# Kernel optimization log

Measured on AMD Instinct MI355X. Metric: run time of the kernel, lower is better.

Reference implementation:

```python
import jax, jax.numpy as jnp
import numpy as np

N_NODES = 8192
N_EDGES = 262144
D_IN = 512
D_OUT = 512


def setup_inputs() -> dict:
    key = jax.random.key(0)
    k1, k2, k3 = jax.random.split(key, 3)
    x = jax.random.normal(k1, (N_NODES, D_IN), dtype=jnp.float32)
    edge_index = jax.random.randint(k2, (2, N_EDGES), 0, N_NODES, dtype=jnp.int64)
    weight = jax.random.normal(k3, (D_IN, D_OUT), dtype=jnp.float32)
    bias = jnp.zeros((D_OUT,), dtype=jnp.float32)
    return {"x": x, "edge_index": edge_index, "weight": weight, "bias": bias}


def reference(x, edge_index, weight, bias):
    # GCN layer with selfloop=True branch of the original module.
    n = x.shape[0]
    # Dense symmetric adjacency via scatter-set, matching adj[ei0,ei1]=1; adj[ei1,ei0]=1
    adj = jnp.zeros((n, n), dtype=x.dtype)
    adj = adj.at[edge_index[0], edge_index[1]].set(1.0)
    adj = adj.at[edge_index[1], edge_index[0]].set(1.0)
    # Add self loops, symmetric degree normalization D^{-1/2} A D^{-1/2}
    adj = adj + jnp.eye(n, dtype=x.dtype)
    deg = jnp.sum(adj, axis=1)
    dinv = 1.0 / jnp.sqrt(deg)
    adj = adj * dinv[:, None] * dinv[None, :]  # == D @ adj @ D (diagonal scaling)
    return adj @ (x @ weight) + bias
```

## Files before the change

### kernel.cpp

```cpp
#include <hip/hip_runtime.h>
#include <hip/hip_bf16.h>


#define ELL_STRIDE 128

typedef __attribute__((ext_vector_type(8))) short bf16x8;
typedef __attribute__((ext_vector_type(4))) float f32x4;

__device__ __forceinline__ unsigned short f2bf(float f) {
  unsigned u = __float_as_uint(f);
  u = (u + 0x7fff + ((u >> 16) & 1)) >> 16;
  return (unsigned short)u;
}
__device__ __forceinline__ float bflo(unsigned u) {
  return __uint_as_float(u << 16);
}
__device__ __forceinline__ float bfhi(unsigned u) {
  return __uint_as_float(u & 0xffff0000u);
}

__global__ __launch_bounds__(256) void fused_front_kernel(
    const int* __restrict__ ei, unsigned* __restrict__ mask, int n_edges,
    int words,
    const float* __restrict__ x, unsigned short* __restrict__ xb, int n4,
    const float* __restrict__ W, unsigned short* __restrict__ Wt, int K, int N,
    unsigned short* __restrict__ Hs, float* __restrict__ dinv, int n_nodes,
    int edge_blocks, int cast_blocks, int tr_blocks) {
  const int bid = blockIdx.x;
  if (bid < edge_blocks) {
    const int e = bid * 256 + threadIdx.x;
    if (e < n_edges) {
      const int u = ei[e];
      const int v = ei[e + n_edges];
      atomicOr(&mask[(size_t)u * words + (v >> 5)], 1u << (v & 31));
      atomicOr(&mask[(size_t)v * words + (u >> 5)], 1u << (u & 31));
    }
    return;
  }
  if (bid < edge_blocks + cast_blocks) {
    const int t = (bid - edge_blocks) * 256 + threadIdx.x;
    if (t < n4) {
      float4 v = ((const float4*)x)[t];
      ushort4 o;
      o.x = f2bf(v.x); o.y = f2bf(v.y); o.z = f2bf(v.z); o.w = f2bf(v.w);
      ((ushort4*)xb)[t] = o;
    }
    return;
  }
  if (bid < edge_blocks + cast_blocks + tr_blocks) {
    __shared__ float tile[32][33];
    const int b = bid - edge_blocks - cast_blocks;
    const int bx = b & ((N >> 5) - 1);
    const int by = b >> (31 - __builtin_clz(N >> 5));
    const int tx = threadIdx.x & 31;
    const int ty = threadIdx.x >> 5;
#pragma unroll
    for (int r = 0; r < 4; ++r)
      tile[ty + 8 * r][tx] = W[(size_t)(by * 32 + ty + 8 * r) * N + bx * 32 + tx];
    __syncthreads();
#pragma unroll
    for (int r = 0; r < 4; ++r)
      Wt[(size_t)(bx * 32 + ty + 8 * r) * K + by * 32 + tx] =
          f2bf(tile[tx][ty + 8 * r]);
    return;
  }
  {
    const int t = threadIdx.x;
    if (t < (N >> 1)) ((unsigned*)(Hs + (size_t)n_nodes * N))[t] = 0;
    if (t == 0) dinv[n_nodes] = 0.f;
  }
}

__global__ __launch_bounds__(256) void fused_mid_kernel(
    const unsigned short* __restrict__ xb,
    const unsigned short* __restrict__ Wt,
    unsigned short* __restrict__ Hs,
    const unsigned* __restrict__ mask, unsigned short* __restrict__ ell,
    int* __restrict__ deg, float* __restrict__ dinv,
    int M, int N, int K, int words, int gemm_blocks, int nbx_sh) {
  __shared__ unsigned short As[512 * 8];
  __shared__ unsigned short Bs[512 * 8];

  const int tid = threadIdx.x;
  const int bid = blockIdx.x;

  if (bid < gemm_blocks) {
    const int wave = tid >> 6;
    const int lane = tid & 63;
    const int q = lane >> 4;
    const int c = lane & 15;
    const int bx = bid & ((1 << nbx_sh) - 1);
    const int by = bid >> nbx_sh;
    const int m0 = by * 64;
    const int n0 = bx * 64;
    const int wr = wave >> 1, wc = wave & 1;

    f32x4 acc[2][2] = {};

    for (int k0 = 0; k0 < K; k0 += 64) {
#pragma unroll
      for (int t = 0; t < 2; ++t) {
        const int sbase = t * 256 + wave * 64;
        const int s = sbase + lane;
        const unsigned short* g =
            xb + (size_t)(m0 + (s & 63)) * K + k0 + (s >> 6) * 8;
        __builtin_amdgcn_global_load_lds(
            (const __attribute__((address_space(1))) void*)g,
            (__attribute__((address_space(3))) void*)(As + sbase * 8), 16, 0, 0);
      }
#pragma unroll
      for (int t = 0; t < 2; ++t) {
        const int sbase = t * 256 + wave * 64;
        const int s = sbase + lane;
        const unsigned short* g =
            Wt + (size_t)(n0 + (s >> 3)) * K + k0 + (s & 7) * 8;
        __builtin_amdgcn_global_load_lds(
            (const __attribute__((address_space(1))) void*)g,
            (__attribute__((address_space(3))) void*)(Bs + sbase * 8), 16, 0, 0);
      }
      __syncthreads();

#pragma unroll
      for (int kk = 0; kk < 2; ++kk) {
        bf16x8 a[2], b[2];
#pragma unroll
        for (int tm = 0; tm < 2; ++tm) {
          const int row = wr * 32 + tm * 16 + c;
          a[tm] = *(const bf16x8*)(As + (((kk * 4 + q) * 64) + row) * 8);
        }
#pragma unroll
        for (int tn = 0; tn < 2; ++tn) {
          const int n = wc * 32 + tn * 16 + c;
          b[tn] = *(const bf16x8*)(Bs + (n * 8 + kk * 4 + q) * 8);
        }
#pragma unroll
        for (int tm = 0; tm < 2; ++tm)
#pragma unroll
          for (int tn = 0; tn < 2; ++tn)
            acc[tm][tn] = __builtin_amdgcn_mfma_f32_16x16x32_bf16(
                a[tm], b[tn], acc[tm][tn], 0, 0, 0);
      }
      __syncthreads();
    }

#pragma unroll
    for (int tm = 0; tm < 2; ++tm) {
#pragma unroll
      for (int r = 0; r < 4; ++r) {
        const int grow = m0 + wr * 32 + tm * 16 + q * 4 + r;
#pragma unroll
        for (int tn = 0; tn < 2; ++tn) {
          const int gcol = n0 + wc * 32 + tn * 16 + c;
          Hs[(size_t)grow * N + gcol] = f2bf(acc[tm][tn][r]);
        }
      }
    }
    return;
  }

  {
    const int wave = tid >> 6, lane = tid & 63;
    const int node = (bid - gemm_blocks) * 4 + wave;
    const unsigned* __restrict__ row = mask + (size_t)node * words;
    unsigned short* __restrict__ out = ell + (size_t)node * ELL_STRIDE;

    int running = 0;
    for (int r = 0; r < words; r += 64) {
      const int w = r + lane;
      unsigned bits = row[w];
      const int cnt = __popc(bits);
      int x = cnt;
#pragma unroll
      for (int d = 1; d < 64; d <<= 1) {
        int y = __shfl_up(x, d, 64);
        if (lane >= d) x += y;
      }
      int pos = running + x - cnt;
      while (bits) {
        const int b = __builtin_ctz(bits);
        bits &= bits - 1;
        if (pos < ELL_STRIDE) out[pos] = (unsigned short)((w << 5) + b);
        ++pos;
      }
      running += __shfl(x, 63, 64);
    }
    for (int p = running + lane; p < ELL_STRIDE; p += 64)
      out[p] = (unsigned short)(p == running ? node : M);
    if (lane == 0) {
      const int dd = running + 1;
      deg[node] = dd < ELL_STRIDE ? dd : ELL_STRIDE;
      dinv[node] = rsqrtf((float)running + 1.0f);
    }
  }
}

__global__ __launch_bounds__(256) void spmm_kernel(
    const unsigned short* __restrict__ ell, const int* __restrict__ deg,
    const float* __restrict__ dinv, const unsigned short* __restrict__ Hs,
    const float* __restrict__ bias, float* __restrict__ out, int n, int D) {
  __shared__ uint2 ji[4][ELL_STRIDE];
  const int wave = threadIdx.x >> 6, lane = threadIdx.x & 63;
  const int i = blockIdx.x * 4 + wave;
  const int h = blockIdx.y;
  const int side = lane >> 5, hl = lane & 31;
  const int Dh = D >> 1;

  {
    const unsigned j0 = ell[(size_t)i * ELL_STRIDE + lane];
    const unsigned j1 = ell[(size_t)i * ELL_STRIDE + 64 + lane];
    ji[wave][lane] = make_uint2(j0, __float_as_uint(dinv[j0]));
    ji[wave][64 + lane] = make_uint2(j1, __float_as_uint(dinv[j1]));
  }
  const int d = deg[i];
  const float di = dinv[i];
  const int kmax = (d + 1) & ~1;

  const unsigned short* __restrict__ hb = Hs + h * Dh + hl * 8;
  float acc[8] = {0.f, 0.f, 0.f, 0.f, 0.f, 0.f, 0.f, 0.f};

#pragma unroll 8
  for (int k = 0; k < kmax; k += 2) {
    const uint2 e = ji[wave][k + side];
    const int j = e.x;
    const float dj = __uint_as_float(e.y);
    const uint4 hv = *(const uint4*)(hb + (size_t)j * D);
    acc[0] += dj * bflo(hv.x); acc[1] += dj * bfhi(hv.x);
    acc[2] += dj * bflo(hv.y); acc[3] += dj * bfhi(hv.y);
    acc[4] += dj * bflo(hv.z); acc[5] += dj * bfhi(hv.z);
    acc[6] += dj * bflo(hv.w); acc[7] += dj * bfhi(hv.w);
  }
#pragma unroll
  for (int t = 0; t < 8; ++t) acc[t] += __shfl_xor(acc[t], 32, 64);

  if (side == 0) {
    const float4 b0 = *(const float4*)(bias + h * Dh + hl * 8);
    const float4 b1 = *(const float4*)(bias + h * Dh + hl * 8 + 4);
    float* op = out + (size_t)i * D + h * Dh + hl * 8;
    float4 o0, o1;
    o0.x = di * acc[0] + b0.x; o0.y = di * acc[1] + b0.y;
    o0.z = di * acc[2] + b0.z; o0.w = di * acc[3] + b0.w;
    o1.x = di * acc[4] + b1.x; o1.y = di * acc[5] + b1.y;
    o1.z = di * acc[6] + b1.z; o1.w = di * acc[7] + b1.w;
    *(float4*)op = o0;
    *(float4*)(op + 4) = o1;
  }
}

extern "C" void kernel_launch(void* const* d_in, const int* in_sizes, int n_in,
                              void* d_out, int out_size, void* d_ws, size_t ws_size,
                              hipStream_t stream) {
  const float* x    = (const float*)d_in[0];
  const int*   ei   = (const int*)d_in[1];
  const float* W    = (const float*)d_in[2];
  const float* bias = (const float*)d_in[3];
  float* out = (float*)d_out;

  const int d_out_dim = in_sizes[3];
  const int d_in_dim  = in_sizes[2] / d_out_dim;
  const int n_nodes   = in_sizes[0] / d_in_dim;
  const int n_edges   = in_sizes[1] / 2;
  const int words     = (n_nodes + 31) / 32;

  char* ws = (char*)d_ws;
  size_t off = 0;
  unsigned* mask = (unsigned*)(ws + off); off += (size_t)n_nodes * words * 4;
  int* deg       = (int*)(ws + off);      off += (size_t)n_nodes * 4;
  float* dinv    = (float*)(ws + off);    off += (size_t)(n_nodes + 1) * 4;
  unsigned short* ell = (unsigned short*)(ws + off); off += (size_t)n_nodes * ELL_STRIDE * 2;
  unsigned short* xb  = (unsigned short*)(ws + off); off += (size_t)n_nodes * d_in_dim * 2;
  unsigned short* Wt  = (unsigned short*)(ws + off); off += (size_t)d_in_dim * d_out_dim * 2;
  unsigned short* Hs  = (unsigned short*)(ws + off);
  off += (size_t)(n_nodes + 1) * d_out_dim * 2;

  hipMemsetAsync(mask, 0, (size_t)n_nodes * words * 4, stream);

  const int edge_blocks = (n_edges + 255) / 256;
  const int n4 = n_nodes * d_in_dim / 4;
  const int cast_blocks = (n4 + 255) / 256;
  const int tr_blocks = (d_in_dim / 32) * (d_out_dim / 32);
  fused_front_kernel<<<edge_blocks + cast_blocks + tr_blocks + 1, 256, 0, stream>>>(
      ei, mask, n_edges, words, x, xb, n4, W, Wt, d_in_dim, d_out_dim,
      Hs, dinv, n_nodes, edge_blocks, cast_blocks, tr_blocks);

  const int nbx = d_out_dim / 64;
  const int nbx_sh = 31 - __builtin_clz(nbx);
  const int gemm_blocks = nbx * (n_nodes / 64);
  const int ell_blocks = n_nodes / 4;
  fused_mid_kernel<<<gemm_blocks + ell_blocks, 256, 0, stream>>>(
      xb, Wt, Hs, mask, ell, deg, dinv,
      n_nodes, d_out_dim, d_in_dim, words, gemm_blocks, nbx_sh);

  dim3 sgrid(n_nodes / 4, 2);
  spmm_kernel<<<sgrid, 256, 0, stream>>>(ell, deg, dinv, Hs, bias, out,
                                         n_nodes, d_out_dim);
}
```

Baseline: 158.7 us.

## Swizzle GEMM B tile in LDS and split SpMM feature dim into eight slices

```diff
diff --git a/kernel.cpp b/kernel.cpp
--- a/kernel.cpp
+++ b/kernel.cpp
@@ -112,8 +112,10 @@
       for (int t = 0; t < 2; ++t) {
         const int sbase = t * 256 + wave * 64;
         const int s = sbase + lane;
+        const int bn = s >> 3;
+        const int bk = (s & 7) ^ (bn & 7);
         const unsigned short* g =
-            Wt + (size_t)(n0 + (s >> 3)) * K + k0 + (s & 7) * 8;
+            Wt + (size_t)(n0 + bn) * K + k0 + bk * 8;
         __builtin_amdgcn_global_load_lds(
             (const __attribute__((address_space(1))) void*)g,
             (__attribute__((address_space(3))) void*)(Bs + sbase * 8), 16, 0, 0);
@@ -131,7 +133,7 @@
 #pragma unroll
         for (int tn = 0; tn < 2; ++tn) {
           const int n = wc * 32 + tn * 16 + c;
-          b[tn] = *(const bf16x8*)(Bs + (n * 8 + kk * 4 + q) * 8);
+          b[tn] = *(const bf16x8*)(Bs + (n * 8 + ((kk * 4 + q) ^ (n & 7))) * 8);
         }
 #pragma unroll
         for (int tm = 0; tm < 2; ++tm)
@@ -200,10 +202,11 @@
     const float* __restrict__ bias, float* __restrict__ out, int n, int D) {
   __shared__ uint2 ji[4][ELL_STRIDE];
   const int wave = threadIdx.x >> 6, lane = threadIdx.x & 63;
-  const int i = blockIdx.x * 4 + wave;
-  const int h = blockIdx.y;
-  const int side = lane >> 5, hl = lane & 31;
-  const int Dh = D >> 1;
+  const int slice = blockIdx.x & 7;
+  const int grp = blockIdx.x >> 3;
+  const int i = grp * 4 + wave;
+  const int e = lane >> 3, c = lane & 7;
+  const int Ds = D >> 3;
 
   {
     const unsigned j0 = ell[(size_t)i * ELL_STRIDE + lane];
@@ -213,16 +216,16 @@
   }
   const int d = deg[i];
   const float di = dinv[i];
-  const int kmax = (d + 1) & ~1;
-
-  const unsigned short* __restrict__ hb = Hs + h * Dh + hl * 8;
+  const int kmax = (d + 7) & ~7;
+
+  const unsigned short* __restrict__ hb = Hs + slice * Ds + c * 8;
   float acc[8] = {0.f, 0.f, 0.f, 0.f, 0.f, 0.f, 0.f, 0.f};
 
-#pragma unroll 8
-  for (int k = 0; k < kmax; k += 2) {
-    const uint2 e = ji[wave][k + side];
-    const int j = e.x;
-    const float dj = __uint_as_float(e.y);
+#pragma unroll 4
+  for (int k = 0; k < kmax; k += 8) {
+    const uint2 t = ji[wave][k + e];
+    const int j = t.x;
+    const float dj = __uint_as_float(t.y);
     const uint4 hv = *(const uint4*)(hb + (size_t)j * D);
     acc[0] += dj * bflo(hv.x); acc[1] += dj * bfhi(hv.x);
     acc[2] += dj * bflo(hv.y); acc[3] += dj * bfhi(hv.y);
@@ -230,12 +233,16 @@
     acc[6] += dj * bflo(hv.w); acc[7] += dj * bfhi(hv.w);
   }
 #pragma unroll
-  for (int t = 0; t < 8; ++t) acc[t] += __shfl_xor(acc[t], 32, 64);
-
-  if (side == 0) {
-    const float4 b0 = *(const float4*)(bias + h * Dh + hl * 8);
-    const float4 b1 = *(const float4*)(bias + h * Dh + hl * 8 + 4);
-    float* op = out + (size_t)i * D + h * Dh + hl * 8;
+  for (int t = 0; t < 8; ++t) {
+    acc[t] += __shfl_xor(acc[t], 8, 64);
+    acc[t] += __shfl_xor(acc[t], 16, 64);
+    acc[t] += __shfl_xor(acc[t], 32, 64);
+  }
+
+  if (lane < 8) {
+    const float4 b0 = *(const float4*)(bias + slice * Ds + lane * 8);
+    const float4 b1 = *(const float4*)(bias + slice * Ds + lane * 8 + 4);
+    float* op = out + (size_t)i * D + slice * Ds + lane * 8;
     float4 o0, o1;
     o0.x = di * acc[0] + b0.x; o0.y = di * acc[1] + b0.y;
     o0.z = di * acc[2] + b0.z; o0.w = di * acc[3] + b0.w;
@@ -290,7 +297,7 @@
       xb, Wt, Hs, mask, ell, deg, dinv,
       n_nodes, d_out_dim, d_in_dim, words, gemm_blocks, nbx_sh);
 
-  dim3 sgrid(n_nodes / 4, 2);
-  spmm_kernel<<<sgrid, 256, 0, stream>>>(ell, deg, dinv, Hs, bias, out,
-                                         n_nodes, d_out_dim);
-}
+  const int spmm_blocks = 8 * (n_nodes / 4);
+  spmm_kernel<<<spmm_blocks, 256, 0, stream>>>(ell, deg, dinv, Hs, bias, out,
+                                               n_nodes, d_out_dim);
+}
```

Result: slower. 169.6 us (+6.8%).

## Swizzle GEMM B tile in LDS and make SpMM wave cover full row

Applied to the files above, without the earlier changes.

```diff
diff --git a/kernel.cpp b/kernel.cpp
--- a/kernel.cpp
+++ b/kernel.cpp
@@ -112,8 +112,10 @@
       for (int t = 0; t < 2; ++t) {
         const int sbase = t * 256 + wave * 64;
         const int s = sbase + lane;
+        const int bn = s >> 3;
+        const int bk = (s & 7) ^ (bn & 7);
         const unsigned short* g =
-            Wt + (size_t)(n0 + (s >> 3)) * K + k0 + (s & 7) * 8;
+            Wt + (size_t)(n0 + bn) * K + k0 + bk * 8;
         __builtin_amdgcn_global_load_lds(
             (const __attribute__((address_space(1))) void*)g,
             (__attribute__((address_space(3))) void*)(Bs + sbase * 8), 16, 0, 0);
@@ -131,7 +133,7 @@
 #pragma unroll
         for (int tn = 0; tn < 2; ++tn) {
           const int n = wc * 32 + tn * 16 + c;
-          b[tn] = *(const bf16x8*)(Bs + (n * 8 + kk * 4 + q) * 8);
+          b[tn] = *(const bf16x8*)(Bs + (n * 8 + ((kk * 4 + q) ^ (n & 7))) * 8);
         }
 #pragma unroll
         for (int tm = 0; tm < 2; ++tm)
@@ -201,49 +203,42 @@
   __shared__ uint2 ji[4][ELL_STRIDE];
   const int wave = threadIdx.x >> 6, lane = threadIdx.x & 63;
   const int i = blockIdx.x * 4 + wave;
-  const int h = blockIdx.y;
-  const int side = lane >> 5, hl = lane & 31;
-  const int Dh = D >> 1;
+  const unsigned rowbytes = (unsigned)(D * 2);
 
   {
     const unsigned j0 = ell[(size_t)i * ELL_STRIDE + lane];
     const unsigned j1 = ell[(size_t)i * ELL_STRIDE + 64 + lane];
-    ji[wave][lane] = make_uint2(j0, __float_as_uint(dinv[j0]));
-    ji[wave][64 + lane] = make_uint2(j1, __float_as_uint(dinv[j1]));
+    ji[wave][lane] = make_uint2(j0 * rowbytes, __float_as_uint(dinv[j0]));
+    ji[wave][64 + lane] = make_uint2(j1 * rowbytes, __float_as_uint(dinv[j1]));
   }
   const int d = deg[i];
   const float di = dinv[i];
-  const int kmax = (d + 1) & ~1;
-
-  const unsigned short* __restrict__ hb = Hs + h * Dh + hl * 8;
+  const int kmax = (d + 7) & ~7;
+
+  const char* __restrict__ hb = (const char*)(Hs + lane * 8);
   float acc[8] = {0.f, 0.f, 0.f, 0.f, 0.f, 0.f, 0.f, 0.f};
 
 #pragma unroll 8
-  for (int k = 0; k < kmax; k += 2) {
-    const uint2 e = ji[wave][k + side];
-    const int j = e.x;
+  for (int k = 0; k < kmax; ++k) {
+    const uint2 e = ji[wave][k];
     const float dj = __uint_as_float(e.y);
-    const uint4 hv = *(const uint4*)(hb + (size_t)j * D);
+    const uint4 hv = *(const uint4*)(hb + e.x);
     acc[0] += dj * bflo(hv.x); acc[1] += dj * bfhi(hv.x);
     acc[2] += dj * bflo(hv.y); acc[3] += dj * bfhi(hv.y);
     acc[4] += dj * bflo(hv.z); acc[5] += dj * bfhi(hv.z);
     acc[6] += dj * bflo(hv.w); acc[7] += dj * bfhi(hv.w);
   }
-#pragma unroll
-  for (int t = 0; t < 8; ++t) acc[t] += __shfl_xor(acc[t], 32, 64);
-
-  if (side == 0) {
-    const float4 b0 = *(const float4*)(bias + h * Dh + hl * 8);
-    const float4 b1 = *(const float4*)(bias + h * Dh + hl * 8 + 4);
-    float* op = out + (size_t)i * D + h * Dh + hl * 8;
-    float4 o0, o1;
-    o0.x = di * acc[0] + b0.x; o0.y = di * acc[1] + b0.y;
-    o0.z = di * acc[2] + b0.z; o0.w = di * acc[3] + b0.w;
-    o1.x = di * acc[4] + b1.x; o1.y = di * acc[5] + b1.y;
-    o1.z = di * acc[6] + b1.z; o1.w = di * acc[7] + b1.w;
-    *(float4*)op = o0;
-    *(float4*)(op + 4) = o1;
-  }
+
+  const float4 b0 = *(const float4*)(bias + lane * 8);
+  const float4 b1 = *(const float4*)(bias + lane * 8 + 4);
+  float* op = out + (size_t)i * D + lane * 8;
+  float4 o0, o1;
+  o0.x = di * acc[0] + b0.x; o0.y = di * acc[1] + b0.y;
+  o0.z = di * acc[2] + b0.z; o0.w = di * acc[3] + b0.w;
+  o1.x = di * acc[4] + b1.x; o1.y = di * acc[5] + b1.y;
+  o1.z = di * acc[6] + b1.z; o1.w = di * acc[7] + b1.w;
+  *(float4*)op = o0;
+  *(float4*)(op + 4) = o1;
 }
 
 extern "C" void kernel_launch(void* const* d_in, const int* in_sizes, int n_in,
@@ -290,7 +285,6 @@
       xb, Wt, Hs, mask, ell, deg, dinv,
       n_nodes, d_out_dim, d_in_dim, words, gemm_blocks, nbx_sh);
 
-  dim3 sgrid(n_nodes / 4, 2);
-  spmm_kernel<<<sgrid, 256, 0, stream>>>(ell, deg, dinv, Hs, bias, out,
-                                         n_nodes, d_out_dim);
-}
+  spmm_kernel<<<n_nodes / 4, 256, 0, stream>>>(ell, deg, dinv, Hs, bias, out,
+                                               n_nodes, d_out_dim);
+}
```

Result: no change. 160.6 us (+1.2%).
